# Optimization experiments

Hardware: AMD Instinct MI355X
Metric: run time of the kernel (lower is better)

The kernel has to match this reference:

```python
import math
import jax, jax.numpy as jnp
import numpy as np

DRAGON_ITERATIONS = 12
DRAGON_SMOOTHING = 0.1


def _dragon_patterns(iterations=DRAGON_ITERATIONS, smoothing=DRAGON_SMOOTHING):
    """Deterministic (non-learned) Dragon curve patterns, matching torch impl."""
    patterns = [np.array([0.5], dtype=np.float32)]
    kernel = np.ones(3, dtype=np.float32) / 3.0
    for _ in range(1, iterations):
        prev = patterns[-1]
        n = len(prev)
        newp = np.zeros(2 * n + 1, dtype=np.float32)
        newp[:n] = prev
        newp[n] = 0.5
        newp[n + 1:] = 1.0 - prev[::-1]
        if smoothing > 0:
            # conv1d with kernel_size=3, padding=1 (zero pad) == np.convolve 'same'
            newp = np.convolve(newp, kernel, mode='same').astype(np.float32)
        newp = (newp - newp.min()) / (newp.max() - newp.min() + 1e-8)
        patterns.append(newp.astype(np.float32))
    return patterns

_PATTERNS = _dragon_patterns()


def _interp_pattern(seq_len):
    """Linearly interpolate selected dragon pattern to seq_len (static shapes)."""
    it = min(int(math.log2(seq_len)), DRAGON_ITERATIONS - 1)
    pattern = _PATTERNS[it]
    if len(pattern) == seq_len:
        w = pattern.copy()
    else:
        x_old = np.linspace(0.0, 1.0, len(pattern), dtype=np.float64)
        x_new = np.linspace(0.0, 1.0, seq_len, dtype=np.float64)
        w = np.interp(x_new, x_old, pattern.astype(np.float64)).astype(np.float32)
    return it, jnp.asarray(w)


def setup_inputs() -> dict:
    key = jax.random.key(0)
    ks = jax.random.split(key, 8)
    B, S, D = 8, 2048, 512
    query = jax.random.normal(ks[0], (B, S, D), dtype=jnp.float32)
    k = jax.random.normal(ks[1], (B, S, D), dtype=jnp.float32)
    value = jax.random.normal(ks[2], (B, S, D), dtype=jnp.float32)
    pattern_scale = jnp.ones((DRAGON_ITERATIONS,), dtype=jnp.float32)
    pattern_bias = jnp.zeros((DRAGON_ITERATIONS,), dtype=jnp.float32)
    w1 = jax.random.normal(ks[3], (DRAGON_ITERATIONS, 64), dtype=jnp.float32) * (1.0 / math.sqrt(DRAGON_ITERATIONS))
    b1 = jnp.zeros((64,), dtype=jnp.float32)
    w2 = jax.random.normal(ks[4], (64, 1), dtype=jnp.float32) * (1.0 / 8.0)
    b2 = jnp.zeros((1,), dtype=jnp.float32)
    return {"query": query, "key": k, "value": value,
            "pattern_scale": pattern_scale, "pattern_bias": pattern_bias,
            "w1": w1, "b1": b1, "w2": w2, "b2": b2}


def reference(query, key, value, pattern_scale, pattern_bias, w1, b1, w2, b2):
    B, S, D = key.shape
    it, base_w = _interp_pattern(S)
    # learned affine + softplus on dragon weights
    dragon_w = jax.nn.softplus(base_w * pattern_scale[it] + pattern_bias[it])  # [S]
    weighted_keys = key * dragon_w[None, :, None]                              # [B,S,D]
    scores = jnp.einsum('bqd,bkd->bqk', query, weighted_keys) / math.sqrt(D)   # [B,S,S]
    attn = jax.nn.softmax(scores, axis=-1)
    # blend factor from one-hot iteration features through tiny MLP
    feat = jax.nn.one_hot(it, DRAGON_ITERATIONS, dtype=query.dtype)            # [12]
    h = jax.nn.relu(feat @ w1 + b1)
    blend = jax.nn.sigmoid(h @ w2 + b2)                                        # [1]
    blend = blend[0]
    final_attn = blend * attn + (1.0 - blend) / S                              # uniform blend
    out = jnp.einsum('bqk,bkd->bqd', final_attn, value)                        # [B,S,D]
    # original does output.squeeze(1); S>1 so it's a no-op here
    return out
```

## Files before the change

kernel.cpp:

```cpp
#include <hip/hip_runtime.h>
#include <cstdint>

#define DEV __device__ __forceinline__

typedef float f32x4 __attribute__((ext_vector_type(4)));
typedef short s16x8 __attribute__((ext_vector_type(8)));

DEV unsigned short f2bf(float f){
    unsigned u = __builtin_bit_cast(unsigned, f);
    u = u + 0x7fffu + ((u >> 16) & 1u);
    return (unsigned short)(u >> 16);
}
DEV float bf2f(unsigned short h){
    unsigned u = ((unsigned)h) << 16;
    return __builtin_bit_cast(float, u);
}

typedef const void __attribute__((address_space(1)))* gcp;
typedef void __attribute__((address_space(3)))* lp;
DEV void gload_lds16(const void* g, void* l){
    __builtin_amdgcn_global_load_lds((gcp)g, (lp)l, 16, 0, 0);
}

__global__ __launch_bounds__(256) void k_stage1(
    const float* __restrict__ Q, const float* __restrict__ V,
    const float* __restrict__ scale, const float* __restrict__ bias,
    const float* __restrict__ w1, const float* __restrict__ b1,
    const float* __restrict__ w2, const float* __restrict__ b2,
    float* __restrict__ dragon_w, float* __restrict__ blend_out,
    unsigned short* __restrict__ Qb, unsigned short* __restrict__ Vt,
    float* __restrict__ vmean_part)
{
    __shared__ float sh[8704];
    int tid = threadIdx.x;
    int bx  = blockIdx.x;

    if (bx == 0){
        float* A    = sh;
        float* Bb   = sh + 4096;
        float* sred = sh + 8192;
        if (tid == 0) A[0] = 0.5f;
        __syncthreads();
        int len = 1;
        for (int it = 1; it < 12; ++it){
            int n = len, nl = 2*n + 1;
            for (int i = tid; i < nl; i += 256){
                float v;
                if (i < n)       v = A[i];
                else if (i == n) v = 0.5f;
                else             v = 1.0f - A[2*n - i];
                Bb[i] = v;
            }
            __syncthreads();
            const float third = 1.0f/3.0f;
            for (int i = tid; i < nl; i += 256){
                float s = Bb[i]*third;
                if (i > 0)    s += Bb[i-1]*third;
                if (i < nl-1) s += Bb[i+1]*third;
                A[i] = s;
            }
            __syncthreads();
            float mn = 3.4e38f, mx = -3.4e38f;
            for (int i = tid; i < nl; i += 256){ float v = A[i]; mn = fminf(mn,v); mx = fmaxf(mx,v); }
            sred[tid] = mn; sred[256 + tid] = mx;
            __syncthreads();
            for (int off = 128; off > 0; off >>= 1){
                if (tid < off){
                    sred[tid]       = fminf(sred[tid],       sred[tid+off]);
                    sred[256 + tid] = fmaxf(sred[256 + tid], sred[256 + tid + off]);
                }
                __syncthreads();
            }
            float lo = sred[0], den = sred[256] - lo + 1e-8f;
            for (int i = tid; i < nl; i += 256) A[i] = (A[i] - lo) / den;
            len = nl;
            __syncthreads();
        }
        float sc = scale[11], bi = bias[11];
        for (int i = tid; i < 2048; i += 256){
            float x = A[2*i]*sc + bi;
            dragon_w[i] = fmaxf(x, 0.f) + log1pf(__expf(-fabsf(x)));
        }
        if (tid < 64){
            float h = fmaxf(w1[11*64 + tid] + b1[tid], 0.f);
            float c = h * w2[tid];
            for (int off = 32; off > 0; off >>= 1) c += __shfl_xor(c, off, 64);
            if (tid == 0) blend_out[0] = 1.f/(1.f + __expf(-(c + b2[0])));
        }
        return;
    }

    if (bx <= 2048){
        const long long total4 = (long long)8*2048*512/4;
        long long stride = 2048LL*256;
        for (long long i = (long long)(bx-1)*256 + tid; i < total4; i += stride){
            long long base = i*4;
            const float4 q = *(const float4*)(Q + base);
            ushort4 qo;
            qo.x = f2bf(q.x); qo.y = f2bf(q.y); qo.z = f2bf(q.z); qo.w = f2bf(q.w);
            *(ushort4*)(Qb + base) = qo;
        }
        return;
    }

    int t = bx - 2049;
    int stile = t & 31, dtile = (t >> 5) & 7, b = t >> 8;
    int s0 = stile*64, d0 = dtile*64;
    float (*tile)[66] = (float(*)[66])sh;
    float* red = sh + 4352;
    int tx = tid & 63, ty = tid >> 6;
    const float* src = V + ((long long)b*2048 + s0)*512 + d0;
    #pragma unroll
    for (int r = 0; r < 16; ++r){
        int row = r*4 + ty;
        tile[row][tx] = src[(long long)row*512 + tx];
    }
    __syncthreads();
    unsigned short* dst = Vt + ((long long)b*512 + d0)*2048 + s0;
    #pragma unroll
    for (int r = 0; r < 16; ++r){
        int drow = r*4 + ty;
        dst[(long long)drow*2048 + tx] = f2bf(tile[tx][drow]);
    }
    int dcol = tid & 63, sp = tid >> 6;
    float s = 0.f;
    #pragma unroll
    for (int ii = 0; ii < 16; ++ii) s += tile[sp*16 + ii][dcol];
    red[sp*64 + dcol] = s;
    __syncthreads();
    if (sp == 0){
        float tot = red[dcol] + red[64+dcol] + red[128+dcol] + red[192+dcol];
        vmean_part[stile*4096 + b*512 + d0 + dcol] = tot * (1.0f/2048.0f);
    }
}

__global__ __launch_bounds__(256) void k_stage2(
    const float* __restrict__ K, const float* __restrict__ dragon_w,
    const float* __restrict__ vmean_part,
    unsigned short* __restrict__ Kb, float* __restrict__ vmean)
{
    int bx = blockIdx.x, tid = threadIdx.x;
    if (bx < 16){
        int idx = bx*256 + tid;
        float s = 0.f;
        #pragma unroll
        for (int st = 0; st < 32; ++st) s += vmean_part[st*4096 + idx];
        vmean[idx] = s;
        return;
    }
    const long long total4 = (long long)8*2048*512/4;
    long long stride = 2048LL*256;
    for (long long i = (long long)(bx-16)*256 + tid; i < total4; i += stride){
        long long base = i*4;
        int s = (int)((base >> 9) & 2047);
        float w = dragon_w[s];
        const float4 k = *(const float4*)(K + base);
        ushort4 ko;
        ko.x = f2bf(k.x*w); ko.y = f2bf(k.y*w); ko.z = f2bf(k.z*w); ko.w = f2bf(k.w*w);
        *(ushort4*)(Kb + base) = ko;
    }
}

#define SCALE_QK 0.04419417382415922f

__global__ __launch_bounds__(256) void k_gemm_qk(
    const unsigned short* __restrict__ Qb, const unsigned short* __restrict__ Kb,
    unsigned short* __restrict__ Sp)
{
    __shared__ unsigned short At[128*64];
    __shared__ unsigned short Bt[128*64];
    int tid = threadIdx.x;
    int lane = tid & 63, wave = tid >> 6;
    int wm = wave >> 1, wn = wave & 1;
    int ln = lane & 15, q4 = lane >> 4;
    int sx = ln & 7;
    int q0 = blockIdx.y*128, k0 = blockIdx.x*128, b = blockIdx.z;
    const unsigned short* Abase = Qb + ((long long)b*2048 + q0)*512;
    const unsigned short* Bbase = Kb + ((long long)b*2048 + k0)*512;

    f32x4 acc[4][4];
    #pragma unroll
    for (int i = 0; i < 4; ++i)
        #pragma unroll
        for (int j = 0; j < 4; ++j) acc[i][j] = (f32x4)0.0f;

    int cc = lane & 7;
    int rg = lane >> 3;
    for (int kt = 0; kt < 8; ++kt){
        #pragma unroll
        for (int c = 0; c < 4; ++c){
            int chunk = wave*4 + c;
            int row = chunk*8 + rg;
            int gc  = cc ^ (row & 7);
            gload_lds16(Abase + (long long)row*512 + kt*64 + gc*8, &At[chunk*512]);
            gload_lds16(Bbase + (long long)row*512 + kt*64 + gc*8, &Bt[chunk*512]);
        }
        __syncthreads();
        #pragma unroll
        for (int ks = 0; ks < 2; ++ks){
            s16x8 af[4], bfr[4];
            int cs = ((ks*4 + q4) ^ sx) * 8;
            #pragma unroll
            for (int i = 0; i < 4; ++i)
                af[i] = *(const s16x8*)&At[(wm*64 + i*16 + ln)*64 + cs];
            #pragma unroll
            for (int j = 0; j < 4; ++j)
                bfr[j] = *(const s16x8*)&Bt[(wn*64 + j*16 + ln)*64 + cs];
            #pragma unroll
            for (int i = 0; i < 4; ++i)
                #pragma unroll
                for (int j = 0; j < 4; ++j)
                    acc[i][j] = __builtin_amdgcn_mfma_f32_16x16x32_bf16(af[i], bfr[j], acc[i][j], 0, 0, 0);
        }
        __syncthreads();
    }
    unsigned short* outp = Sp + (long long)b*2048*2048;
    #pragma unroll
    for (int i = 0; i < 4; ++i){
        #pragma unroll
        for (int j = 0; j < 4; ++j){
            #pragma unroll
            for (int r = 0; r < 4; ++r){
                int q = q0 + wm*64 + i*16 + q4*4 + r;
                int k = k0 + wn*64 + j*16 + ln;
                float v = __expf(acc[i][j][r] * SCALE_QK);
                outp[(long long)q*2048 + k] = f2bf(v);
            }
        }
    }
}

__global__ __launch_bounds__(256) void k_gemm_pv(
    const unsigned short* __restrict__ Sp, const unsigned short* __restrict__ Vt,
    const float* __restrict__ vmean, const float* __restrict__ blendp,
    float* __restrict__ out)
{
    __shared__ unsigned short At[128*64];
    __shared__ unsigned short Bt[128*64];
    __shared__ float l_sh[128];
    int tid = threadIdx.x;
    int lane = tid & 63, wave = tid >> 6;
    int wm = wave >> 1, wn = wave & 1;
    int ln = lane & 15, q4 = lane >> 4;
    int sx = ln & 7;
    int q0 = blockIdx.y*128, d0 = blockIdx.x*128, b = blockIdx.z;
    const unsigned short* Abase = Sp + (long long)b*2048*2048 + (long long)q0*2048;
    const unsigned short* Bbase = Vt + ((long long)b*512 + d0)*2048;

    f32x4 acc[4][4];
    #pragma unroll
    for (int i = 0; i < 4; ++i)
        #pragma unroll
        for (int j = 0; j < 4; ++j) acc[i][j] = (f32x4)0.0f;
    float lsum[4] = {0.f, 0.f, 0.f, 0.f};

    int cc = lane & 7;
    int rg = lane >> 3;
    for (int kt = 0; kt < 32; ++kt){
        #pragma unroll
        for (int c = 0; c < 4; ++c){
            int chunk = wave*4 + c;
            int row = chunk*8 + rg;
            int gc  = cc ^ (row & 7);
            gload_lds16(Abase + (long long)row*2048 + kt*64 + gc*8, &At[chunk*512]);
            gload_lds16(Bbase + (long long)row*2048 + kt*64 + gc*8, &Bt[chunk*512]);
        }
        __syncthreads();
        #pragma unroll
        for (int ks = 0; ks < 2; ++ks){
            s16x8 af[4], bfr[4];
            int cs = ((ks*4 + q4) ^ sx) * 8;
            #pragma unroll
            for (int i = 0; i < 4; ++i)
                af[i] = *(const s16x8*)&At[(wm*64 + i*16 + ln)*64 + cs];
            #pragma unroll
            for (int j = 0; j < 4; ++j)
                bfr[j] = *(const s16x8*)&Bt[(wn*64 + j*16 + ln)*64 + cs];
            if (wn == 0){
                #pragma unroll
                for (int i = 0; i < 4; ++i){
                    float s = 0.f;
                    #pragma unroll
                    for (int jj = 0; jj < 8; ++jj) s += bf2f((unsigned short)af[i][jj]);
                    lsum[i] += s;
                }
            }
            #pragma unroll
            for (int i = 0; i < 4; ++i)
                #pragma unroll
                for (int j = 0; j < 4; ++j)
                    acc[i][j] = __builtin_amdgcn_mfma_f32_16x16x32_bf16(af[i], bfr[j], acc[i][j], 0, 0, 0);
        }
        __syncthreads();
    }
    if (wn == 0){
        #pragma unroll
        for (int i = 0; i < 4; ++i){
            float v = lsum[i];
            v += __shfl_xor(v, 16, 64);
            v += __shfl_xor(v, 32, 64);
            if (lane < 16) l_sh[wm*64 + i*16 + lane] = v;
        }
    }
    __syncthreads();

    float blend = blendp[0];
    float ib = 1.0f - blend;
    float* obase = out + ((long long)b*2048 + q0)*512 + d0;
    float vm[4];
    #pragma unroll
    for (int j = 0; j < 4; ++j) vm[j] = vmean[b*512 + d0 + wn*64 + j*16 + ln];
    #pragma unroll
    for (int i = 0; i < 4; ++i){
        #pragma unroll
        for (int r = 0; r < 4; ++r){
            int ql = wm*64 + i*16 + q4*4 + r;
            float linv = 1.0f / l_sh[ql];
            #pragma unroll
            for (int j = 0; j < 4; ++j){
                int dl = wn*64 + j*16 + ln;
                obase[(long long)ql*512 + dl] = blend*acc[i][j][r]*linv + ib*vm[j];
            }
        }
    }
}

extern "C" void kernel_launch(void* const* d_in, const int* in_sizes, int n_in,
                              void* d_out, int out_size, void* d_ws, size_t ws_size,
                              hipStream_t stream)
{
    (void)in_sizes; (void)n_in; (void)out_size; (void)ws_size;
    const float* Q  = (const float*)d_in[0];
    const float* K  = (const float*)d_in[1];
    const float* V  = (const float*)d_in[2];
    const float* ps = (const float*)d_in[3];
    const float* pb = (const float*)d_in[4];
    const float* w1 = (const float*)d_in[5];
    const float* b1 = (const float*)d_in[6];
    const float* w2 = (const float*)d_in[7];
    const float* b2 = (const float*)d_in[8];
    float* out = (float*)d_out;

    char* ws = (char*)d_ws;
    float* dragon_w        = (float*)(ws);
    float* blend           = (float*)(ws + 8192);
    float* vmean           = (float*)(ws + 16384);
    float* vmean_part      = (float*)(ws + 32768);
    size_t off = 32768 + (size_t)512*1024;
    unsigned short* Qb     = (unsigned short*)(ws + off);
    unsigned short* Kb     = (unsigned short*)(ws + off + (size_t)16*1024*1024);
    unsigned short* Vt     = (unsigned short*)(ws + off + (size_t)32*1024*1024);
    unsigned short* Sp     = (unsigned short*)(ws + off + (size_t)48*1024*1024);

    hipLaunchKernelGGL(k_stage1,  dim3(4097),      dim3(256), 0, stream,
                       Q, V, ps, pb, w1, b1, w2, b2, dragon_w, blend, Qb, Vt, vmean_part);
    hipLaunchKernelGGL(k_stage2,  dim3(2064),      dim3(256), 0, stream,
                       K, dragon_w, vmean_part, Kb, vmean);
    hipLaunchKernelGGL(k_gemm_qk, dim3(16, 16, 8), dim3(256), 0, stream,
                       Qb, Kb, Sp);
    hipLaunchKernelGGL(k_gemm_pv, dim3(4, 16, 8),  dim3(256), 0, stream,
                       Sp, Vt, vmean, blend, out);
}
```

Before: 254.5 us.

## Restructure prep stages: single-block dragon kernel, fused Q/K/V conversion pass

Splits the dragon-pattern/blend computation into a tiny one-block kernel that uses wave-shuffle reductions and folds normalization into the next iteration. Q and K bf16 conversion then run in one fused pass alongside the V transpose, replacing the old two-kernel prep where K conversion ran separately. The vmean partial reduction moves into a few QK GEMM blocks. The aim is fewer passes over the prep work and a shorter serial dragon chain. The cost is a single-block serial kernel on the critical path and extra work in some GEMM blocks.

```diff
diff --git a/kernel.cpp b/kernel.cpp
--- a/kernel.cpp
+++ b/kernel.cpp
@@ -22,92 +22,101 @@
     __builtin_amdgcn_global_load_lds((gcp)g, (lp)l, 16, 0, 0);
 }
 
-__global__ __launch_bounds__(256) void k_stage1(
-    const float* __restrict__ Q, const float* __restrict__ V,
+__global__ __launch_bounds__(256) void k_prep(
     const float* __restrict__ scale, const float* __restrict__ bias,
     const float* __restrict__ w1, const float* __restrict__ b1,
     const float* __restrict__ w2, const float* __restrict__ b2,
-    float* __restrict__ dragon_w, float* __restrict__ blend_out,
-    unsigned short* __restrict__ Qb, unsigned short* __restrict__ Vt,
-    float* __restrict__ vmean_part)
-{
-    __shared__ float sh[8704];
+    float* __restrict__ dragon_w, float* __restrict__ blend_out)
+{
+    __shared__ float A[4095];
+    __shared__ float Bb[4095];
+    __shared__ float red[8];
+    int tid = threadIdx.x;
+    int lane = tid & 63, w = tid >> 6;
+
+    if (tid == 0) A[0] = 0.5f;
+    __syncthreads();
+    float lo = 0.f, rden = 1.f;
+    int len = 1;
+    const float third = 1.0f/3.0f;
+    for (int it = 1; it < 12; ++it){
+        int n = len, nl = 2*n + 1;
+        for (int i = tid; i < nl; i += 256){
+            float v;
+            if (i < n)       v = (A[i] - lo) * rden;
+            else if (i == n) v = 0.5f;
+            else             v = 1.0f - (A[2*n - i] - lo) * rden;
+            Bb[i] = v;
+        }
+        __syncthreads();
+        float mn = 3.4e38f, mx = -3.4e38f;
+        for (int i = tid; i < nl; i += 256){
+            float s = Bb[i];
+            if (i > 0)    s += Bb[i-1];
+            if (i < nl-1) s += Bb[i+1];
+            s *= third;
+            A[i] = s;
+            mn = fminf(mn, s); mx = fmaxf(mx, s);
+        }
+        #pragma unroll
+        for (int off = 32; off > 0; off >>= 1){
+            mn = fminf(mn, __shfl_xor(mn, off, 64));
+            mx = fmaxf(mx, __shfl_xor(mx, off, 64));
+        }
+        if (lane == 0){ red[w] = mn; red[4 + w] = mx; }
+        __syncthreads();
+        mn = fminf(fminf(red[0], red[1]), fminf(red[2], red[3]));
+        mx = fmaxf(fmaxf(red[4], red[5]), fmaxf(red[6], red[7]));
+        lo = mn; rden = 1.0f / (mx - mn + 1e-8f);
+        len = nl;
+        __syncthreads();
+    }
+    float sc = scale[11], bi = bias[11];
+    for (int i = tid; i < 2048; i += 256){
+        float x = (A[2*i] - lo) * rden * sc + bi;
+        dragon_w[i] = fmaxf(x, 0.f) + log1pf(__expf(-fabsf(x)));
+    }
+    if (tid < 64){
+        float h = fmaxf(w1[11*64 + tid] + b1[tid], 0.f);
+        float c = h * w2[tid];
+        for (int off = 32; off > 0; off >>= 1) c += __shfl_xor(c, off, 64);
+        if (tid == 0) blend_out[0] = 1.f/(1.f + __expf(-(c + b2[0])));
+    }
+}
+
+__global__ __launch_bounds__(256) void k_conv(
+    const float* __restrict__ Q, const float* __restrict__ K,
+    const float* __restrict__ V, const float* __restrict__ dragon_w,
+    unsigned short* __restrict__ Qb, unsigned short* __restrict__ Kb,
+    unsigned short* __restrict__ Vt, float* __restrict__ vmean_part)
+{
+    __shared__ float sh[4480];
     int tid = threadIdx.x;
     int bx  = blockIdx.x;
 
-    if (bx == 0){
-        float* A    = sh;
-        float* Bb   = sh + 4096;
-        float* sred = sh + 8192;
-        if (tid == 0) A[0] = 0.5f;
-        __syncthreads();
-        int len = 1;
-        for (int it = 1; it < 12; ++it){
-            int n = len, nl = 2*n + 1;
-            for (int i = tid; i < nl; i += 256){
-                float v;
-                if (i < n)       v = A[i];
-                else if (i == n) v = 0.5f;
-                else             v = 1.0f - A[2*n - i];
-                Bb[i] = v;
-            }
-            __syncthreads();
-            const float third = 1.0f/3.0f;
-            for (int i = tid; i < nl; i += 256){
-                float s = Bb[i]*third;
-                if (i > 0)    s += Bb[i-1]*third;
-                if (i < nl-1) s += Bb[i+1]*third;
-                A[i] = s;
-            }
-            __syncthreads();
-            float mn = 3.4e38f, mx = -3.4e38f;
-            for (int i = tid; i < nl; i += 256){ float v = A[i]; mn = fminf(mn,v); mx = fmaxf(mx,v); }
-            sred[tid] = mn; sred[256 + tid] = mx;
-            __syncthreads();
-            for (int off = 128; off > 0; off >>= 1){
-                if (tid < off){
-                    sred[tid]       = fminf(sred[tid],       sred[tid+off]);
-                    sred[256 + tid] = fmaxf(sred[256 + tid], sred[256 + tid + off]);
-                }
-                __syncthreads();
-            }
-            float lo = sred[0], den = sred[256] - lo + 1e-8f;
-            for (int i = tid; i < nl; i += 256) A[i] = (A[i] - lo) / den;
-            len = nl;
-            __syncthreads();
-        }
-        float sc = scale[11], bi = bias[11];
-        for (int i = tid; i < 2048; i += 256){
-            float x = A[2*i]*sc + bi;
-            dragon_w[i] = fmaxf(x, 0.f) + log1pf(__expf(-fabsf(x)));
-        }
-        if (tid < 64){
-            float h = fmaxf(w1[11*64 + tid] + b1[tid], 0.f);
-            float c = h * w2[tid];
-            for (int off = 32; off > 0; off >>= 1) c += __shfl_xor(c, off, 64);
-            if (tid == 0) blend_out[0] = 1.f/(1.f + __expf(-(c + b2[0])));
+    if (bx < 1024){
+        const long long total4 = (long long)8*2048*512/4;
+        long long stride = 1024LL*256;
+        for (long long i = (long long)bx*256 + tid; i < total4; i += stride){
+            long long base = i*4;
+            int s = (int)((base >> 9) & 2047);
+            float wv = dragon_w[s];
+            const float4 q = *(const float4*)(Q + base);
+            const float4 k = *(const float4*)(K + base);
+            ushort4 qo, ko;
+            qo.x = f2bf(q.x);    qo.y = f2bf(q.y);    qo.z = f2bf(q.z);    qo.w = f2bf(q.w);
+            ko.x = f2bf(k.x*wv); ko.y = f2bf(k.y*wv); ko.z = f2bf(k.z*wv); ko.w = f2bf(k.w*wv);
+            *(ushort4*)(Qb + base) = qo;
+            *(ushort4*)(Kb + base) = ko;
         }
         return;
     }
 
-    if (bx <= 2048){
-        const long long total4 = (long long)8*2048*512/4;
-        long long stride = 2048LL*256;
-        for (long long i = (long long)(bx-1)*256 + tid; i < total4; i += stride){
-            long long base = i*4;
-            const float4 q = *(const float4*)(Q + base);
-            ushort4 qo;
-            qo.x = f2bf(q.x); qo.y = f2bf(q.y); qo.z = f2bf(q.z); qo.w = f2bf(q.w);
-            *(ushort4*)(Qb + base) = qo;
-        }
-        return;
-    }
-
-    int t = bx - 2049;
+    int t = bx - 1024;
     int stile = t & 31, dtile = (t >> 5) & 7, b = t >> 8;
     int s0 = stile*64, d0 = dtile*64;
     float (*tile)[66] = (float(*)[66])sh;
-    float* red = sh + 4352;
+    float* red = sh + 4224;
     int tx = tid & 63, ty = tid >> 6;
     const float* src = V + ((long long)b*2048 + s0)*512 + d0;
     #pragma unroll
@@ -134,37 +143,11 @@
     }
 }
 
-__global__ __launch_bounds__(256) void k_stage2(
-    const float* __restrict__ K, const float* __restrict__ dragon_w,
-    const float* __restrict__ vmean_part,
-    unsigned short* __restrict__ Kb, float* __restrict__ vmean)
-{
-    int bx = blockIdx.x, tid = threadIdx.x;
-    if (bx < 16){
-        int idx = bx*256 + tid;
-        float s = 0.f;
-        #pragma unroll
-        for (int st = 0; st < 32; ++st) s += vmean_part[st*4096 + idx];
-        vmean[idx] = s;
-        return;
-    }
-    const long long total4 = (long long)8*2048*512/4;
-    long long stride = 2048LL*256;
-    for (long long i = (long long)(bx-16)*256 + tid; i < total4; i += stride){
-        long long base = i*4;
-        int s = (int)((base >> 9) & 2047);
-        float w = dragon_w[s];
-        const float4 k = *(const float4*)(K + base);
-        ushort4 ko;
-        ko.x = f2bf(k.x*w); ko.y = f2bf(k.y*w); ko.z = f2bf(k.z*w); ko.w = f2bf(k.w*w);
-        *(ushort4*)(Kb + base) = ko;
-    }
-}
-
 #define SCALE_QK 0.04419417382415922f
 
 __global__ __launch_bounds__(256) void k_gemm_qk(
     const unsigned short* __restrict__ Qb, const unsigned short* __restrict__ Kb,
+    const float* __restrict__ vmean_part, float* __restrict__ vmean,
     unsigned short* __restrict__ Sp)
 {
     __shared__ unsigned short At[128*64];
@@ -175,6 +158,18 @@
     int ln = lane & 15, q4 = lane >> 4;
     int sx = ln & 7;
     int q0 = blockIdx.y*128, k0 = blockIdx.x*128, b = blockIdx.z;
+
+    if (blockIdx.x == 0 && blockIdx.y == 0){
+        #pragma unroll
+        for (int rep = 0; rep < 2; ++rep){
+            int idx = b*512 + rep*256 + tid;
+            float s = 0.f;
+            #pragma unroll
+            for (int st = 0; st < 32; ++st) s += vmean_part[st*4096 + idx];
+            vmean[idx] = s;
+        }
+    }
+
     const unsigned short* Abase = Qb + ((long long)b*2048 + q0)*512;
     const unsigned short* Bbase = Kb + ((long long)b*2048 + k0)*512;
 
@@ -352,12 +347,12 @@
     unsigned short* Vt     = (unsigned short*)(ws + off + (size_t)32*1024*1024);
     unsigned short* Sp     = (unsigned short*)(ws + off + (size_t)48*1024*1024);
 
-    hipLaunchKernelGGL(k_stage1,  dim3(4097),      dim3(256), 0, stream,
-                       Q, V, ps, pb, w1, b1, w2, b2, dragon_w, blend, Qb, Vt, vmean_part);
-    hipLaunchKernelGGL(k_stage2,  dim3(2064),      dim3(256), 0, stream,
-                       K, dragon_w, vmean_part, Kb, vmean);
+    hipLaunchKernelGGL(k_prep,    dim3(1),         dim3(256), 0, stream,
+                       ps, pb, w1, b1, w2, b2, dragon_w, blend);
+    hipLaunchKernelGGL(k_conv,    dim3(3072),      dim3(256), 0, stream,
+                       Q, K, V, dragon_w, Qb, Kb, Vt, vmean_part);
     hipLaunchKernelGGL(k_gemm_qk, dim3(16, 16, 8), dim3(256), 0, stream,
-                       Qb, Kb, Sp);
+                       Qb, Kb, vmean_part, vmean, Sp);
     hipLaunchKernelGGL(k_gemm_pv, dim3(4, 16, 8),  dim3(256), 0, stream,
                        Sp, Vt, vmean, blend, out);
 }
```

Result: slower. 269.9 us (+6.1%).
